# Kernel optimization log

Measured on AMD Instinct MI355X. Metric: run time of the kernel, lower is better.

Reference implementation:

```python
import jax, jax.numpy as jnp
import numpy as np

GAMMA_EXP = 1.0 / 2.2
PATTERN = 'RGGB'
H, W = 3072, 4096


def _conv1d(x, k, axis):
    """Cross-correlation of 2D x with 1D kernel k along axis, reflect padding
    (matches torch F.conv2d on reflect-padded input)."""
    p = (len(k) - 1) // 2
    pad = [(p, p) if a == axis else (0, 0) for a in range(2)]
    xp = jnp.pad(x, pad, mode='reflect')
    n = x.shape[axis]
    out = jnp.zeros_like(x)
    for i, ki in enumerate(k):
        if ki == 0.0:
            continue
        sl = [slice(None), slice(None)]
        sl[axis] = slice(i, i + n)
        out = out + ki * xp[tuple(sl)]
    return out


def _bayer_masks(shape, pattern):
    ch = {c: np.zeros((2, 2), np.float32) for c in 'RGB'}
    for i, c in enumerate(pattern):
        ch[c][i // 2, i % 2] = 1.0
    reps = ((shape[0] + 1) // 2, (shape[1] + 1) // 2)
    return tuple(jnp.asarray(np.tile(ch[c], reps)[:shape[0], :shape[1]]) for c in 'RGB')


def _shift_left2(x, axis):
    # pad by 2 on the far side with reflect, then drop first 2 -> x[j+2] with reflect at border
    pad = [(0, 2) if a == axis else (0, 0) for a in range(2)]
    xp = jnp.pad(x, pad, mode='reflect')
    sl = [slice(None), slice(None)]
    sl[axis] = slice(2, None)
    return xp[tuple(sl)]


def _menon2007(CFA, pattern):
    R_m, G_m, B_m = _bayer_masks(CFA.shape, pattern)
    h0 = [0.0, 0.5, 0.0, 0.5, 0.0]
    h1 = [-0.25, 0.0, 0.5, 0.0, -0.25]

    R = CFA * R_m
    G = CFA * G_m
    B = CFA * B_m

    G_H = jnp.where(G_m == 0, _conv1d(CFA, h0, 1) + _conv1d(CFA, h1, 1), G)
    G_V = jnp.where(G_m == 0, _conv1d(CFA, h0, 0) + _conv1d(CFA, h1, 0), G)

    C_H = jnp.where(R_m == 1, R - G_H, 0.0)
    C_H = jnp.where(B_m == 1, B - G_H, C_H)
    C_V = jnp.where(R_m == 1, R - G_V, 0.0)
    C_V = jnp.where(B_m == 1, B - G_V, C_V)

    D_H = jnp.abs(C_H - _shift_left2(C_H, axis=1))
    D_V = jnp.abs(C_V - _shift_left2(C_V, axis=0))

    k_row = [0.0, 0.0, 3.0, 0.0, 3.0]   # k[2, :]
    k_col = [1.0, 0.0, 3.0, 0.0, 1.0]   # k[:, 2]
    d_H = _conv1d(D_H, k_row, 1) + _conv1d(D_H, k_col, 0) - D_H * 3.0
    d_V = _conv1d(D_V, k_row, 1) + _conv1d(D_V, k_col, 0) - D_V * 3.0

    M = (d_V >= d_H).astype(CFA.dtype)
    G = jnp.where(G_m == 1, G, M * G_H + (1.0 - M) * G_V)

    R_r = jnp.any(R_m == 1, axis=1, keepdims=True) & jnp.ones_like(R_m, bool)
    B_r = jnp.any(B_m == 1, axis=1, keepdims=True) & jnp.ones_like(B_m, bool)
    kb = [0.5, 0.0, 0.5]

    R = jnp.where((G_m == 1) & R_r, G + _conv1d(R, kb, 1) - _conv1d(G, kb, 1), R)
    R = jnp.where((G_m == 1) & B_r, G + _conv1d(R, kb, 0) - _conv1d(G, kb, 0), R)
    B = jnp.where((G_m == 1) & B_r, G + _conv1d(B, kb, 1) - _conv1d(G, kb, 1), B)
    B = jnp.where((G_m == 1) & R_r, G + _conv1d(B, kb, 0) - _conv1d(G, kb, 0), B)

    R_at_B = M * (B + _conv1d(R, kb, 1) - _conv1d(B, kb, 1)) \
           + (1.0 - M) * (B + _conv1d(R, kb, 0) - _conv1d(B, kb, 0))
    R = jnp.where(B_r & (B_m == 1), R_at_B, R)

    B_at_R = M * (R + _conv1d(B, kb, 1) - _conv1d(R, kb, 1)) \
           + (1.0 - M) * (R + _conv1d(B, kb, 0) - _conv1d(R, kb, 0))
    B = jnp.where(R_r & (R_m == 1), B_at_R, B)

    return jnp.stack([R, G, B], axis=0)


def setup_inputs() -> dict:
    key = jax.random.key(0)
    k1, _ = jax.random.split(key)
    raw = jax.random.uniform(k1, (H, W), dtype=jnp.float32)
    wb = jnp.array([1.6, 1.2, 1.4], dtype=jnp.float32).reshape(3, 1, 1)
    return {"raw": raw, "wb": wb}


def reference(raw, wb):
    scaled = raw.astype(jnp.float32) / 65535.0
    rgb = _menon2007(scaled, PATTERN)
    rgb = rgb * wb
    rgb = jnp.clip(rgb, 0.0, 1.0)
    mn = jnp.min(rgb)
    mx = jnp.max(rgb)
    rng = mx - mn
    rgb = jnp.where(rng > 1e-6, (rgb - mn) / jnp.maximum(rng, 1e-12), rgb)
    rgb = jnp.power(jnp.maximum(rgb, 1e-12), GAMMA_EXP)
    return rgb
```

## Files before the change

### kernel.cpp

```cpp
#include <hip/hip_runtime.h>
#include <hip/hip_bf16.h>
#include <hip/hip_fp16.h>

#pragma clang fp contract(off)

constexpr int IMG_H = 3072;
constexpr int IMG_W = 4096;
constexpr int TS = 32;
constexpr float GAMMA_E = (float)(1.0 / 2.2);
constexpr float SC = 1048576.0f;
constexpr float INV_SC = 1.0f / SC;

__device__ __forceinline__ int mir(int v, int n) {
    v = (v < 0) ? -v : v;
    return (v >= n) ? (2 * n - 2 - v) : v;
}

constexpr int CFA_STR = 44, GH_STR = 40, GV_STR = 40, DH_STR = 40, DV_STR = 40,
              G_STR = 36, HV_STR = 36;
constexpr int OFF_CFA = 0;
constexpr int OFF_GH  = OFF_CFA + 46*44;
constexpr int OFF_GV  = OFF_GH  + 40*40;
constexpr int OFF_DH  = OFF_GV  + 42*40;
constexpr int OFF_DV  = OFF_DH  + 40*40;
constexpr int OFF_G   = OFF_DV  + 40*40;
constexpr int SMEM_N  = OFF_G   + 36*36;
constexpr int OFF_HH  = OFF_DH;
constexpr int OFF_VV  = OFF_DV;

__global__ void init_slots(unsigned int* slots) {
    int t = threadIdx.x;
    if (t < 512) slots[t] = (t < 256) ? 0x7F800000u : 0u;
}

__device__ __forceinline__ float pack_gm(float g, unsigned mb) {
    return __uint_as_float((__float_as_uint(g) & ~1u) | mb);
}

template <bool FP16>
__global__ __launch_bounds__(256) void demosaic_pass1(
    const float* __restrict__ raw, const float* __restrict__ wb,
    float* __restrict__ out, __half* __restrict__ hout,
    unsigned int* __restrict__ slots)
{
    __shared__ __align__(16) float sm[SMEM_N];
    __shared__ float redmn[4], redmx[4];
    const int tid = threadIdx.x;
    const int gr0 = blockIdx.y * TS;
    const int gc0 = blockIdx.x * TS;
    const bool fast = (blockIdx.x != 0) && (blockIdx.x != gridDim.x - 1) &&
                      (blockIdx.y != 0) && (blockIdx.y != gridDim.y - 1);

    if (fast) {
        const float* src = raw + (long long)(gr0 - 6) * IMG_W + (gc0 - 4);
        auto doLoad = [&](int ar, int q) {
            float4 v = *(const float4*)(src + ar * IMG_W + (q << 2));
            *(float4*)&sm[OFF_CFA + ar * CFA_STR + (q << 2)] =
                make_float4(v.x / 65535.0f, v.y / 65535.0f, v.z / 65535.0f, v.w / 65535.0f);
        };
        for (int i = tid; i < 368; i += 256) doLoad(i >> 3, i & 7);
        for (int i = tid; i < 138; i += 256) doLoad(i / 3, 8 + (i % 3));
        __syncthreads();

        auto doGH4 = [&](int ar, int ac4) {
            int cb = OFF_CFA + (ar + 2) * CFA_STR + ac4;
            const float4 a = *(const float4*)&sm[cb];
            const float4 b = *(const float4*)&sm[cb + 4];
            float w[8] = {a.x, a.y, a.z, a.w, b.x, b.y, b.z, b.w};
            float o[4];
#pragma unroll
            for (int j = 0; j < 4; ++j) {
                float x0 = w[j + 2];
                float t0 = 0.5f * w[j + 1] + 0.5f * w[j + 3];
                float t1 = (-0.25f * w[j] + 0.5f * x0) + (-0.25f * w[j + 4]);
                o[j] = ((ar + ac4 + j) & 1) ? x0 : (t0 + t1);
            }
            *(float4*)&sm[OFF_GH + ar * GH_STR + ac4] = make_float4(o[0], o[1], o[2], o[3]);
        };
        for (int i = tid; i < 320; i += 256) doGH4(i >> 3, (i & 7) << 2);
        for (int i = tid; i < 80; i += 256) doGH4(i >> 1, 32 + ((i & 1) << 2));

        auto doGV44 = [&](int rb, int ac4) {
            int r0 = (rb == 10) ? 38 : (rb << 2);
            float col[4][8];
#pragma unroll
            for (int k = 0; k < 8; ++k) {
                int rbase = OFF_CFA + (r0 + k) * CFA_STR + ac4;
                const float4 qa = *(const float4*)&sm[rbase];
                const float4 qb = *(const float4*)&sm[rbase + 4];
                col[0][k] = qa.z; col[1][k] = qa.w; col[2][k] = qb.x; col[3][k] = qb.y;
            }
#pragma unroll
            for (int ii = 0; ii < 4; ++ii) {
                float o[4];
#pragma unroll
                for (int j = 0; j < 4; ++j) {
                    float x0 = col[j][ii + 2];
                    float t0 = 0.5f * col[j][ii + 1] + 0.5f * col[j][ii + 3];
                    float t1 = (-0.25f * col[j][ii] + 0.5f * x0) + (-0.25f * col[j][ii + 4]);
                    o[j] = ((r0 + ii + ac4 + j) & 1) ? x0 : (t0 + t1);
                }
                *(float4*)&sm[OFF_GV + (r0 + ii) * GV_STR + ac4] = make_float4(o[0], o[1], o[2], o[3]);
            }
        };
        for (int i = tid; i < 88; i += 256) doGV44(i >> 3, (i & 7) << 2);
        for (int i = tid; i < 22; i += 256) doGV44(i >> 1, 32 + ((i & 1) << 2));
        __syncthreads();

        auto doD4 = [&](int ar, int ac4) {
            int cb = OFF_CFA + (ar + 2) * CFA_STR + ac4;
            const float4 a = *(const float4*)&sm[cb];
            const float4 b = *(const float4*)&sm[cb + 4];
            float cw[8] = {a.x, a.y, a.z, a.w, b.x, b.y, b.z, b.w};
            int c4b = OFF_CFA + (ar + 4) * CFA_STR + ac4;
            const float4 da = *(const float4*)&sm[c4b];
            const float4 db = *(const float4*)&sm[c4b + 4];
            float cd[4] = {da.z, da.w, db.x, db.y};
            const float4 g0 = *(const float4*)&sm[OFF_GH + ar * GH_STR + ac4];
            const float4 g1 = *(const float4*)&sm[OFF_GH + ar * GH_STR + ac4 + 4];
            float gh[8] = {g0.x, g0.y, g0.z, g0.w, g1.x, g1.y, g1.z, g1.w};
            const float4 v0 = *(const float4*)&sm[OFF_GV + ar * GV_STR + ac4];
            const float4 v2 = *(const float4*)&sm[OFF_GV + (ar + 2) * GV_STR + ac4];
            float gva[4] = {v0.x, v0.y, v0.z, v0.w};
            float gvb[4] = {v2.x, v2.y, v2.z, v2.w};
            float oh[4], ov[4];
#pragma unroll
            for (int j = 0; j < 4; ++j) {
                float aH = cw[j + 2] - gh[j];
                float bH = cw[j + 4] - gh[j + 2];
                oh[j] = fabsf(aH - bH);
                float aV = cw[j + 2] - gva[j];
                float bV = cd[j] - gvb[j];
                ov[j] = fabsf(aV - bV);
            }
            *(float4*)&sm[OFF_DH + ar * DH_STR + ac4] = make_float4(oh[0], oh[1], oh[2], oh[3]);
            *(float4*)&sm[OFF_DV + ar * DV_STR + ac4] = make_float4(ov[0], ov[1], ov[2], ov[3]);
        };
        for (int i = tid; i < 320; i += 256) doD4(i >> 3, (i & 7) << 2);
        for (int i = tid; i < 80; i += 256) doD4(i >> 1, 32 + ((i & 1) << 2));
        __syncthreads();

        auto doMG4 = [&](int ar, int ac4) {
            int hb2 = OFF_DH + (ar + 2) * DH_STR + ac4;
            const float4 h0 = *(const float4*)&sm[hb2];
            const float4 h1 = *(const float4*)&sm[hb2 + 4];
            float hw[8] = {h0.x, h0.y, h0.z, h0.w, h1.x, h1.y, h1.z, h1.w};
            const float4 huq = *(const float4*)&sm[OFF_DH + ar * DH_STR + ac4];
            const float4 hdq = *(const float4*)&sm[OFF_DH + (ar + 4) * DH_STR + ac4];
            int vb2 = OFF_DV + (ar + 2) * DV_STR + ac4;
            const float4 w0 = *(const float4*)&sm[vb2];
            const float4 w1 = *(const float4*)&sm[vb2 + 4];
            float vw[8] = {w0.x, w0.y, w0.z, w0.w, w1.x, w1.y, w1.z, w1.w};
            const float4 vuq = *(const float4*)&sm[OFF_DV + ar * DV_STR + ac4];
            const float4 vdq = *(const float4*)&sm[OFF_DV + (ar + 4) * DV_STR + ac4];
            float hu[4] = {huq.x, huq.y, huq.z, huq.w};
            float hd[4] = {hdq.x, hdq.y, hdq.z, hdq.w};
            float vu[4] = {vuq.x, vuq.y, vuq.z, vuq.w};
            float vd[4] = {vdq.x, vdq.y, vdq.z, vdq.w};
            int cfb = OFF_CFA + (ar + 4) * CFA_STR + ac4;
            const float4 ca = *(const float4*)&sm[cfb];
            const float4 cbq = *(const float4*)&sm[cfb + 4];
            float cf[4] = {ca.z, ca.w, cbq.x, cbq.y};
            const float4 ghq = *(const float4*)&sm[OFF_GH + (ar + 2) * GH_STR + ac4];
            const float4 gvq = *(const float4*)&sm[OFF_GV + (ar + 2) * GV_STR + ac4];
            float gha[4] = {ghq.x, ghq.y, ghq.z, ghq.w};
            float gvv[4] = {gvq.x, gvq.y, gvq.z, gvq.w};
            float o[4];
#pragma unroll
            for (int j = 0; j < 4; ++j) {
                float Dh0 = hw[j];
                float trowH = 3.0f * Dh0 + 3.0f * hw[j + 2];
                float tcolH = (hu[j] + 3.0f * Dh0) + hd[j];
                float dHv = (trowH + tcolH) - 3.0f * Dh0;
                float Dv0 = vw[j];
                float trowV = 3.0f * Dv0 + 3.0f * vw[j + 2];
                float tcolV = (vu[j] + 3.0f * Dv0) + vd[j];
                float dVv = (trowV + tcolV) - 3.0f * Dv0;
                unsigned mb = (dVv >= dHv) ? 1u : 0u;
                float g = ((ar + ac4 + j) & 1) ? cf[j] : (mb ? gha[j] : gvv[j]);
                o[j] = pack_gm(g, mb);
            }
            *(float4*)&sm[OFF_G + ar * G_STR + ac4] = make_float4(o[0], o[1], o[2], o[3]);
        };
        for (int i = tid; i < 288; i += 256) doMG4(i >> 3, (i & 7) << 2);
        for (int i = tid; i < 36; i += 256) doMG4(i, 32);
        __syncthreads();

        auto doHV4 = [&](int ar, int ac4) {
            int gb1 = OFF_G + (ar + 1) * G_STR + ac4;
            const float4 ga = *(const float4*)&sm[gb1];
            const float4 gb2 = *(const float4*)&sm[gb1 + 4];
            float gw[8] = {ga.x, ga.y, ga.z, ga.w, gb2.x, gb2.y, gb2.z, gb2.w};
            int gub = OFF_G + ar * G_STR + ac4;
            const float4 gua = *(const float4*)&sm[gub];
            const float4 gub4 = *(const float4*)&sm[gub + 4];
            float gu[6] = {gua.x, gua.y, gua.z, gua.w, gub4.x, gub4.y};
            int gdb = OFF_G + (ar + 2) * G_STR + ac4;
            const float4 gda = *(const float4*)&sm[gdb];
            const float4 gdb4 = *(const float4*)&sm[gdb + 4];
            float gd[6] = {gda.x, gda.y, gda.z, gda.w, gdb4.x, gdb4.y};
            int c5 = OFF_CFA + (ar + 5) * CFA_STR + ac4;
            const float4 ca = *(const float4*)&sm[c5];
            const float4 cb2 = *(const float4*)&sm[c5 + 4];
            float cw[8] = {ca.x, ca.y, ca.z, ca.w, cb2.x, cb2.y, cb2.z, cb2.w};
            int c4i = OFF_CFA + (ar + 4) * CFA_STR + ac4;
            const float4 cua = *(const float4*)&sm[c4i];
            const float4 cub = *(const float4*)&sm[c4i + 4];
            float cu[8] = {cua.x, cua.y, cua.z, cua.w, cub.x, cub.y, cub.z, cub.w};
            int c6i = OFF_CFA + (ar + 6) * CFA_STR + ac4;
            const float4 cda = *(const float4*)&sm[c6i];
            const float4 cdb = *(const float4*)&sm[c6i + 4];
            float cdn[8] = {cda.x, cda.y, cda.z, cda.w, cdb.x, cdb.y, cdb.z, cdb.w};
            float oh[4], ov[4];
#pragma unroll
            for (int j = 0; j < 4; ++j) {
                float g0 = gw[j + 1];
                oh[j] = g0 + 0.5f * (cw[j + 2] + cw[j + 4] - gw[j] - gw[j + 2]);
                ov[j] = g0 + 0.5f * (cu[j + 3] + cdn[j + 3] - gu[j + 1] - gd[j + 1]);
            }
            *(float4*)&sm[OFF_HH + ar * HV_STR + ac4] = make_float4(oh[0], oh[1], oh[2], oh[3]);
            *(float4*)&sm[OFF_VV + ar * HV_STR + ac4] = make_float4(ov[0], ov[1], ov[2], ov[3]);
        };
        for (int i = tid; i < 272; i += 256) doHV4(i >> 3, (i & 7) << 2);
        for (int i = tid; i < 34; i += 256) doHV4(i, 32);
    } else {
        auto CFA = [&](int r, int c) -> float { return sm[OFF_CFA + (r - gr0 + 6) * CFA_STR + (c - gc0 + 4)]; };
        auto GH  = [&](int r, int c) -> float { return sm[OFF_GH  + (r - gr0 + 4) * GH_STR  + (c - gc0 + 2)]; };
        auto GV  = [&](int r, int c) -> float { return sm[OFF_GV  + (r - gr0 + 4) * GV_STR  + (c - gc0 + 2)]; };
        auto DH  = [&](int r, int c) -> float { return sm[OFF_DH  + (r - gr0 + 4) * DH_STR  + (c - gc0 + 2)]; };
        auto DV  = [&](int r, int c) -> float { return sm[OFF_DV  + (r - gr0 + 4) * DV_STR  + (c - gc0 + 2)]; };
        auto Gg  = [&](int r, int c) -> float { return sm[OFF_G   + (r - gr0 + 2) * G_STR   + (c - gc0 + 2)]; };

        for (int i = tid; i < 46 * 44; i += 256) {
            int ar = i / 44, ac = i % 44;
            int r2 = mir(gr0 + ar - 6, IMG_H), c2 = mir(gc0 + ac - 4, IMG_W);
            sm[OFF_CFA + ar * CFA_STR + ac] = raw[r2 * IMG_W + c2] / 65535.0f;
        }
        __syncthreads();
        for (int i = tid; i < 40 * 40; i += 256) {
            int ar = i / 40, ac = i % 40;
            int r2 = mir(gr0 + ar - 4, IMG_H), c2 = mir(gc0 + ac - 2, IMG_W);
            float x0 = CFA(r2, c2);
            float t0 = 0.5f * CFA(r2, c2 - 1) + 0.5f * CFA(r2, c2 + 1);
            float t1 = (-0.25f * CFA(r2, c2 - 2) + 0.5f * x0) + (-0.25f * CFA(r2, c2 + 2));
            sm[OFF_GH + ar * GH_STR + ac] = (((r2 + c2) & 1) ? x0 : (t0 + t1));
        }
        for (int i = tid; i < 42 * 38; i += 256) {
            int ar = i / 38, ac = i % 38;
            int r2 = mir(gr0 + ar - 4, IMG_H), c2 = mir(gc0 + ac - 2, IMG_W);
            float x0 = CFA(r2, c2);
            float t0 = 0.5f * CFA(r2 - 1, c2) + 0.5f * CFA(r2 + 1, c2);
            float t1 = (-0.25f * CFA(r2 - 2, c2) + 0.5f * x0) + (-0.25f * CFA(r2 + 2, c2));
            sm[OFF_GV + ar * GV_STR + ac] = (((r2 + c2) & 1) ? x0 : (t0 + t1));
        }
        __syncthreads();
        for (int i = tid; i < 40 * 38; i += 256) {
            int ar = i / 38, ac = i % 38;
            int r2 = mir(gr0 + ar - 4, IMG_H), c2 = mir(gc0 + ac - 2, IMG_W);
            float aH = CFA(r2, c2) - GH(r2, c2);
            float bH = CFA(r2, c2 + 2) - GH(r2, c2 + 2);
            float aV = CFA(r2, c2) - GV(r2, c2);
            float bV = CFA(r2 + 2, c2) - GV(r2 + 2, c2);
            sm[OFF_DH + ar * DH_STR + ac] = fabsf(aH - bH);
            sm[OFF_DV + ar * DV_STR + ac] = fabsf(aV - bV);
        }
        __syncthreads();
        for (int i = tid; i < 36 * 36; i += 256) {
            int ar = i / 36, ac = i % 36;
            int r2 = mir(gr0 + ar - 2, IMG_H), c2 = mir(gc0 + ac - 2, IMG_W);
            float Dh0 = DH(r2, c2);
            float trowH = 3.0f * Dh0 + 3.0f * DH(r2, c2 + 2);
            float tcolH = (DH(r2 - 2, c2) + 3.0f * Dh0) + DH(r2 + 2, c2);
            float dHv = (trowH + tcolH) - 3.0f * Dh0;
            float Dv0 = DV(r2, c2);
            float trowV = 3.0f * Dv0 + 3.0f * DV(r2, c2 + 2);
            float tcolV = (DV(r2 - 2, c2) + 3.0f * Dv0) + DV(r2 + 2, c2);
            float dVv = (trowV + tcolV) - 3.0f * Dv0;
            unsigned mb = (dVv >= dHv) ? 1u : 0u;
            float g = ((r2 + c2) & 1) ? CFA(r2, c2) : (mb ? GH(r2, c2) : GV(r2, c2));
            sm[OFF_G + ar * G_STR + ac] = pack_gm(g, mb);
        }
        __syncthreads();
        for (int i = tid; i < 34 * 34; i += 256) {
            int ar = i / 34, ac = i % 34;
            int r2 = mir(gr0 + ar - 1, IMG_H), c2 = mir(gc0 + ac - 1, IMG_W);
            float g0 = Gg(r2, c2);
            float hh = g0 + 0.5f * (CFA(r2, c2 - 1) + CFA(r2, c2 + 1) - Gg(r2, c2 - 1) - Gg(r2, c2 + 1));
            float vv = g0 + 0.5f * (CFA(r2 - 1, c2) + CFA(r2 + 1, c2) - Gg(r2 - 1, c2) - Gg(r2 + 1, c2));
            sm[OFF_HH + ar * HV_STR + ac] = hh;
            sm[OFF_VV + ar * HV_STR + ac] = vv;
        }
    }
    __syncthreads();

    const float wr = wb[0], wg = wb[1], wbv = wb[2];
    const int pr = tid >> 3;
    const int pc0 = (tid & 7) << 2;
    const bool rowOdd = (pr & 1) != 0;
    int hbase = OFF_HH + (pr + 1) * HV_STR + pc0;
    const float4 h1a = *(const float4*)&sm[hbase];
    const float4 h1b = *(const float4*)&sm[hbase + 4];
    float hwc[8] = {h1a.x, h1a.y, h1a.z, h1a.w, h1b.x, h1b.y, h1b.z, h1b.w};
    int vbase = OFF_VV + (pr + 1) * HV_STR + pc0;
    const float4 v1a = *(const float4*)&sm[vbase];
    const float4 v1b = *(const float4*)&sm[vbase + 4];
    float vwc[8] = {v1a.x, v1a.y, v1a.z, v1a.w, v1b.x, v1b.y, v1b.z, v1b.w};
    int hub = OFF_HH + pr * HV_STR + pc0;
    const float4 huA = *(const float4*)&sm[hub];
    const float4 huB = *(const float4*)&sm[hub + 4];
    float hu[6] = {huA.x, huA.y, huA.z, huA.w, huB.x, huB.y};
    int hdb = OFF_HH + (pr + 2) * HV_STR + pc0;
    const float4 hdA = *(const float4*)&sm[hdb];
    const float4 hdB = *(const float4*)&sm[hdb + 4];
    float hd[6] = {hdA.x, hdA.y, hdA.z, hdA.w, hdB.x, hdB.y};
    int vub = OFF_VV + pr * HV_STR + pc0;
    const float4 vuA = *(const float4*)&sm[vub];
    const float4 vuB = *(const float4*)&sm[vub + 4];
    float vu[6] = {vuA.x, vuA.y, vuA.z, vuA.w, vuB.x, vuB.y};
    int vdb = OFF_VV + (pr + 2) * HV_STR + pc0;
    const float4 vdA = *(const float4*)&sm[vdb];
    const float4 vdB = *(const float4*)&sm[vdb + 4];
    float vd[6] = {vdA.x, vdA.y, vdA.z, vdA.w, vdB.x, vdB.y};
    const float4 cfq = *(const float4*)&sm[OFF_CFA + (pr + 6) * CFA_STR + pc0 + 4];
    float cf[4] = {cfq.x, cfq.y, cfq.z, cfq.w};
    int ggb = OFF_G + (pr + 2) * G_STR + pc0;
    const float4 gA = *(const float4*)&sm[ggb];
    const float4 gB = *(const float4*)&sm[ggb + 4];
    float ggr[4] = {gA.z, gA.w, gB.x, gB.y};

    float mn = 1e30f, mx = -1e30f;
    float rr[4], go[4], bo[4];
    __half hR[4], hG[4], hB[4];
#pragma unroll
    for (int j = 0; j < 4; ++j) {
        const float cfa = cf[j];
        const float g = ggr[j];
        const unsigned mb = __float_as_uint(g) & 1u;
        float sH = (hwc[j] - vwc[j]) + (hwc[j + 2] - vwc[j + 2]);
        float sV = (hu[j + 1] - vu[j + 1]) + (hd[j + 1] - vd[j + 1]);
        float X = mb ? (cfa - 0.5f * sH) : (cfa + 0.5f * sV);
        float R, B;
        if ((j & 1) == 0) {
            R = rowOdd ? vwc[j + 1] : cfa;
            B = rowOdd ? hwc[j + 1] : X;
        } else {
            R = rowOdd ? X : hwc[j + 1];
            B = rowOdd ? cfa : vwc[j + 1];
        }
        R = fminf(fmaxf(R * wr, 0.f), 1.f);
        float Gx = fminf(fmaxf(g * wg, 0.f), 1.f);
        B = fminf(fmaxf(B * wbv, 0.f), 1.f);
        if constexpr (FP16) {
            hR[j] = __float2half(R * SC);  R  = __half2float(hR[j]);
            hG[j] = __float2half(Gx * SC); Gx = __half2float(hG[j]);
            hB[j] = __float2half(B * SC);  B  = __half2float(hB[j]);
        }
        mn = fminf(mn, fminf(R, fminf(Gx, B)));
        mx = fmaxf(mx, fmaxf(R, fmaxf(Gx, B)));
        rr[j] = R; go[j] = Gx; bo[j] = B;
    }
    const long long HW = (long long)IMG_H * IMG_W;
    const long long base = (long long)(gr0 + pr) * IMG_W + (gc0 + pc0);
    if constexpr (FP16) {
        auto pack = [](__half a, __half b) {
            __half2 p = __halves2half2(a, b);
            return *reinterpret_cast<unsigned int*>(&p);
        };
        *(uint2*)(hout + base)          = make_uint2(pack(hR[0], hR[1]), pack(hR[2], hR[3]));
        *(uint2*)(hout + HW + base)     = make_uint2(pack(hG[0], hG[1]), pack(hG[2], hG[3]));
        *(uint2*)(hout + 2 * HW + base) = make_uint2(pack(hB[0], hB[1]), pack(hB[2], hB[3]));
    } else {
        *(float4*)(out + base)          = make_float4(rr[0], rr[1], rr[2], rr[3]);
        *(float4*)(out + HW + base)     = make_float4(go[0], go[1], go[2], go[3]);
        *(float4*)(out + 2 * HW + base) = make_float4(bo[0], bo[1], bo[2], bo[3]);
    }

#pragma unroll
    for (int off2 = 32; off2 > 0; off2 >>= 1) {
        mn = fminf(mn, __shfl_xor(mn, off2));
        mx = fmaxf(mx, __shfl_xor(mx, off2));
    }
    if ((tid & 63) == 0) { redmn[tid >> 6] = mn; redmx[tid >> 6] = mx; }
    __syncthreads();
    if (tid == 0) {
        mn = fminf(fminf(redmn[0], redmn[1]), fminf(redmn[2], redmn[3]));
        mx = fmaxf(fmaxf(redmx[0], redmx[1]), fmaxf(redmx[2], redmx[3]));
        if constexpr (FP16) { mn *= INV_SC; mx *= INV_SC; }
        int slot = (int)((blockIdx.y * gridDim.x + blockIdx.x) & 255);
        atomicMin(&slots[slot], __float_as_uint(mn));
        atomicMax(&slots[256 + slot], __float_as_uint(mx));
    }
}

__device__ __forceinline__ void reduce_slots(const unsigned int* slots, int tid,
                                             float* smn, float* smx, float& mn, float& mx) {
    mn = __uint_as_float(slots[tid]);
    mx = __uint_as_float(slots[256 + tid]);
#pragma unroll
    for (int off2 = 32; off2 > 0; off2 >>= 1) {
        mn = fminf(mn, __shfl_xor(mn, off2));
        mx = fmaxf(mx, __shfl_xor(mx, off2));
    }
    if ((tid & 63) == 0) { smn[tid >> 6] = mn; smx[tid >> 6] = mx; }
    __syncthreads();
    mn = fminf(fminf(smn[0], smn[1]), fminf(smn[2], smn[3]));
    mx = fmaxf(fmaxf(smx[0], smx[1]), fmaxf(smx[2], smx[3]));
}

__device__ __forceinline__ float gamma_hw(float a) {
    return __builtin_amdgcn_exp2f(GAMMA_E * __builtin_amdgcn_logf(a));
}

__global__ __launch_bounds__(256) void finalize_pass2_h(
    const __half* __restrict__ hin, float* __restrict__ out,
    const unsigned int* __restrict__ slots)
{
    __shared__ float smn[4], smx[4];
    const int tid = threadIdx.x;
    float mn, mx;
    reduce_slots(slots, tid, smn, smx, mn, mx);
    const float rng = mx - mn;
    const bool app = rng > 1e-6f;
    const float invden = 1.0f / fmaxf(rng, 1e-12f);

    const long long n8 = (long long)3 * IMG_H * IMG_W / 8;
    const uint4* pin = (const uint4*)hin;
    float4* po = (float4*)out;
    for (long long idx = (long long)blockIdx.x * blockDim.x + tid; idx < n8;
         idx += (long long)gridDim.x * blockDim.x) {
        uint4 u = pin[idx];
        float f[8];
        float2 t;
        t = __half22float2(*(__half2*)&u.x); f[0] = t.x; f[1] = t.y;
        t = __half22float2(*(__half2*)&u.y); f[2] = t.x; f[3] = t.y;
        t = __half22float2(*(__half2*)&u.z); f[4] = t.x; f[5] = t.y;
        t = __half22float2(*(__half2*)&u.w); f[6] = t.x; f[7] = t.y;
#pragma unroll
        for (int k = 0; k < 8; ++k) {
            float a = f[k] * INV_SC;
            a = app ? (a - mn) * invden : a;
            f[k] = gamma_hw(fmaxf(a, 1e-12f));
        }
        po[2 * idx]     = make_float4(f[0], f[1], f[2], f[3]);
        po[2 * idx + 1] = make_float4(f[4], f[5], f[6], f[7]);
    }
}

__global__ __launch_bounds__(256) void finalize_pass2_f(
    float* __restrict__ out, const unsigned int* __restrict__ slots)
{
    __shared__ float smn[4], smx[4];
    const int tid = threadIdx.x;
    float mn, mx;
    reduce_slots(slots, tid, smn, smx, mn, mx);
    const float rng = mx - mn;
    const bool app = rng > 1e-6f;
    const float invden = 1.0f / fmaxf(rng, 1e-12f);

    const long long n4 = (long long)3 * IMG_H * IMG_W / 4;
    float4* p = (float4*)out;
    for (long long idx = (long long)blockIdx.x * blockDim.x + tid; idx < n4;
         idx += (long long)gridDim.x * blockDim.x) {
        float4 v = p[idx];
        v.x = gamma_hw(fmaxf(app ? (v.x - mn) * invden : v.x, 1e-12f));
        v.y = gamma_hw(fmaxf(app ? (v.y - mn) * invden : v.y, 1e-12f));
        v.z = gamma_hw(fmaxf(app ? (v.z - mn) * invden : v.z, 1e-12f));
        v.w = gamma_hw(fmaxf(app ? (v.w - mn) * invden : v.w, 1e-12f));
        p[idx] = v;
    }
}

extern "C" void kernel_launch(void* const* d_in, const int* in_sizes, int n_in,
                              void* d_out, int out_size, void* d_ws, size_t ws_size,
                              hipStream_t stream) {
    (void)in_sizes; (void)n_in; (void)out_size;
    const float* raw = (const float*)d_in[0];
    const float* wb = (const float*)d_in[1];
    float* out = (float*)d_out;
    unsigned int* slots = (unsigned int*)d_ws;
    __half* hplanes = (__half*)((char*)d_ws + 4096);
    const size_t need = 4096 + (size_t)3 * IMG_H * IMG_W * sizeof(__half);
    const bool use_fp16 = ws_size >= need;

    init_slots<<<1, 512, 0, stream>>>(slots);
    dim3 grid(IMG_W / TS, IMG_H / TS);
    if (use_fp16) {
        demosaic_pass1<true><<<grid, 256, 0, stream>>>(raw, wb, out, hplanes, slots);
        finalize_pass2_h<<<dim3(2048), 256, 0, stream>>>(hplanes, out, slots);
    } else {
        demosaic_pass1<false><<<grid, 256, 0, stream>>>(raw, wb, out, hplanes, slots);
        finalize_pass2_f<<<dim3(2048), 256, 0, stream>>>(out, slots);
    }
}
```

Baseline: 177.9 us.

## Fuse G_H/G_V into D computation and store only non-green D values

The separate G_H and G_V shared-memory stages are removed. The horizontal and vertical green estimates are recomputed on the fly in the D stage and in the M/G stage, and D_H and D_V are stored only at non-green sites in a half-width layout. This removes two shared arrays and one barrier and shrinks the LDS footprint, with launch bounds requesting 6 blocks per CU for higher occupancy. In exchange it adds redundant arithmetic, plus parity-dependent indexing and more register pressure.

```diff
diff --git a/kernel.cpp b/kernel.cpp
--- a/kernel.cpp
+++ b/kernel.cpp
@@ -16,17 +16,17 @@
     return (v >= n) ? (2 * n - 2 - v) : v;
 }
 
-constexpr int CFA_STR = 44, GH_STR = 40, GV_STR = 40, DH_STR = 40, DV_STR = 40,
-              G_STR = 36, HV_STR = 36;
+constexpr int CFA_STR = 44;
+constexpr int D_STR   = 20;
+constexpr int G_STR   = 36;
+constexpr int HV_STR  = 36;
 constexpr int OFF_CFA = 0;
-constexpr int OFF_GH  = OFF_CFA + 46*44;
-constexpr int OFF_GV  = OFF_GH  + 40*40;
-constexpr int OFF_DH  = OFF_GV  + 42*40;
-constexpr int OFF_DV  = OFF_DH  + 40*40;
-constexpr int OFF_G   = OFF_DV  + 40*40;
-constexpr int SMEM_N  = OFF_G   + 36*36;
+constexpr int OFF_G   = 2024;
+constexpr int OFF_DH  = OFF_G + 36*36;
+constexpr int OFF_DV  = OFF_DH + 40*20;
 constexpr int OFF_HH  = OFF_DH;
-constexpr int OFF_VV  = OFF_DV;
+constexpr int OFF_VV  = OFF_HH + 34*36;
+constexpr int SMEM_N  = OFF_VV + 34*36;
 
 __global__ void init_slots(unsigned int* slots) {
     int t = threadIdx.x;
@@ -38,7 +38,7 @@
 }
 
 template <bool FP16>
-__global__ __launch_bounds__(256) void demosaic_pass1(
+__global__ __launch_bounds__(256, 6) void demosaic_pass1(
     const float* __restrict__ raw, const float* __restrict__ wb,
     float* __restrict__ out, __half* __restrict__ hout,
     unsigned int* __restrict__ slots)
@@ -53,183 +53,212 @@
 
     if (fast) {
         const float* src = raw + (long long)(gr0 - 6) * IMG_W + (gc0 - 4);
-        auto doLoad = [&](int ar, int q) {
-            float4 v = *(const float4*)(src + ar * IMG_W + (q << 2));
-            *(float4*)&sm[OFF_CFA + ar * CFA_STR + (q << 2)] =
+        auto doLoad = [&](int ar, int qd) {
+            float4 v = *(const float4*)(src + ar * IMG_W + (qd << 2));
+            *(float4*)&sm[OFF_CFA + ar * CFA_STR + (qd << 2)] =
                 make_float4(v.x / 65535.0f, v.y / 65535.0f, v.z / 65535.0f, v.w / 65535.0f);
         };
         for (int i = tid; i < 368; i += 256) doLoad(i >> 3, i & 7);
         for (int i = tid; i < 138; i += 256) doLoad(i / 3, 8 + (i % 3));
         __syncthreads();
 
-        auto doGH4 = [&](int ar, int ac4) {
-            int cb = OFF_CFA + (ar + 2) * CFA_STR + ac4;
-            const float4 a = *(const float4*)&sm[cb];
-            const float4 b = *(const float4*)&sm[cb + 4];
-            float w[8] = {a.x, a.y, a.z, a.w, b.x, b.y, b.z, b.w};
-            float o[4];
+        auto doA = [&](int ar, int ku) {
+            const int p = ar & 1;
+            const int cb = OFF_CFA + (ar + 2) * CFA_STR + 8 * ku;
+            float w[16];
+            {
+                const float4 a = *(const float4*)&sm[cb];
+                const float4 b = *(const float4*)&sm[cb + 4];
+                const float4 c = *(const float4*)&sm[cb + 8];
+                const float4 d = *(const float4*)&sm[cb + 12];
+                w[0]=a.x; w[1]=a.y; w[2]=a.z; w[3]=a.w;
+                w[4]=b.x; w[5]=b.y; w[6]=b.z; w[7]=b.w;
+                w[8]=c.x; w[9]=c.y; w[10]=c.z; w[11]=c.w;
+                w[12]=d.x; w[13]=d.y; w[14]=d.z; w[15]=d.w;
+            }
+            float cvj[7][4];
+#pragma unroll
+            for (int k = 0; k < 7; ++k) {
+                if (k == 2) {
+                    cvj[2][0]=w[2+p]; cvj[2][1]=w[4+p]; cvj[2][2]=w[6+p]; cvj[2][3]=w[8+p];
+                    continue;
+                }
+                int rb = OFF_CFA + (ar + k) * CFA_STR + 8 * ku;
+                float2 e  = *(const float2*)&sm[rb + 2];
+                float4 f  = *(const float4*)&sm[rb + 4];
+                float2 g2 = *(const float2*)&sm[rb + 8];
+                if (p == 0) { cvj[k][0]=e.x; cvj[k][1]=f.x; cvj[k][2]=f.z; cvj[k][3]=g2.x; }
+                else        { cvj[k][0]=e.y; cvj[k][1]=f.y; cvj[k][2]=f.w; cvj[k][3]=g2.y; }
+            }
+            auto ghe = [&](int wi) -> float {
+                float x0 = w[wi];
+                float t0 = 0.5f * w[wi-1] + 0.5f * w[wi+1];
+                float t1 = (-0.25f * w[wi-2] + 0.5f * x0) + (-0.25f * w[wi+2]);
+                return t0 + t1;
+            };
+            auto gve = [&](int k0, int j2) -> float {
+                float x0 = cvj[k0][j2];
+                float t0 = 0.5f * cvj[k0-1][j2] + 0.5f * cvj[k0+1][j2];
+                float t1 = (-0.25f * cvj[k0-2][j2] + 0.5f * x0) + (-0.25f * cvj[k0+2][j2]);
+                return t0 + t1;
+            };
+            float dhp[4], dvp[4];
 #pragma unroll
             for (int j = 0; j < 4; ++j) {
-                float x0 = w[j + 2];
-                float t0 = 0.5f * w[j + 1] + 0.5f * w[j + 3];
-                float t1 = (-0.25f * w[j] + 0.5f * x0) + (-0.25f * w[j + 4]);
-                o[j] = ((ar + ac4 + j) & 1) ? x0 : (t0 + t1);
-            }
-            *(float4*)&sm[OFF_GH + ar * GH_STR + ac4] = make_float4(o[0], o[1], o[2], o[3]);
-        };
-        for (int i = tid; i < 320; i += 256) doGH4(i >> 3, (i & 7) << 2);
-        for (int i = tid; i < 80; i += 256) doGH4(i >> 1, 32 + ((i & 1) << 2));
-
-        auto doGV44 = [&](int rb, int ac4) {
-            int r0 = (rb == 10) ? 38 : (rb << 2);
-            float col[4][8];
-#pragma unroll
-            for (int k = 0; k < 8; ++k) {
-                int rbase = OFF_CFA + (r0 + k) * CFA_STR + ac4;
-                const float4 qa = *(const float4*)&sm[rbase];
-                const float4 qb = *(const float4*)&sm[rbase + 4];
-                col[0][k] = qa.z; col[1][k] = qa.w; col[2][k] = qb.x; col[3][k] = qb.y;
-            }
-#pragma unroll
-            for (int ii = 0; ii < 4; ++ii) {
-                float o[4];
-#pragma unroll
-                for (int j = 0; j < 4; ++j) {
-                    float x0 = col[j][ii + 2];
-                    float t0 = 0.5f * col[j][ii + 1] + 0.5f * col[j][ii + 3];
-                    float t1 = (-0.25f * col[j][ii] + 0.5f * x0) + (-0.25f * col[j][ii + 4]);
-                    o[j] = ((r0 + ii + ac4 + j) & 1) ? x0 : (t0 + t1);
+                int wi = 2*j + 2 + p;
+                float gh0 = ghe(wi), gh2 = ghe(wi + 2);
+                float ch0 = w[wi] - gh0, ch2 = w[wi + 2] - gh2;
+                dhp[j] = fabsf(ch0 - ch2);
+                float gv0 = gve(2, j), gv2 = gve(4, j);
+                float cv0 = cvj[2][j] - gv0, cv2 = cvj[4][j] - gv2;
+                dvp[j] = fabsf(cv0 - cv2);
+            }
+            *(float4*)&sm[OFF_DH + ar * D_STR + 4*ku] = make_float4(dhp[0],dhp[1],dhp[2],dhp[3]);
+            *(float4*)&sm[OFF_DV + ar * D_STR + 4*ku] = make_float4(dvp[0],dvp[1],dvp[2],dvp[3]);
+        };
+        for (int i = tid; i < 200; i += 256) doA(i / 5, i % 5);
+        __syncthreads();
+
+        auto doB = [&](int ar, int ku) {
+            const int q = ar & 1;
+            const int k4 = 4 * ku;
+            float hw[6], vw[6], hu[4], hd[4], vu[4], vd[4];
+            {
+                int b0 = OFF_DH + (ar + 2) * D_STR + k4;
+                float4 t = *(const float4*)&sm[b0]; hw[0]=t.x; hw[1]=t.y; hw[2]=t.z; hw[3]=t.w;
+                float2 u = *(const float2*)&sm[b0 + 4]; hw[4]=u.x; hw[5]=u.y;
+                float4 a = *(const float4*)&sm[OFF_DH + ar*D_STR + k4];     hu[0]=a.x; hu[1]=a.y; hu[2]=a.z; hu[3]=a.w;
+                float4 b = *(const float4*)&sm[OFF_DH + (ar+4)*D_STR + k4]; hd[0]=b.x; hd[1]=b.y; hd[2]=b.z; hd[3]=b.w;
+                int v0 = OFF_DV + (ar + 2) * D_STR + k4;
+                float4 t2 = *(const float4*)&sm[v0]; vw[0]=t2.x; vw[1]=t2.y; vw[2]=t2.z; vw[3]=t2.w;
+                float2 u2 = *(const float2*)&sm[v0 + 4]; vw[4]=u2.x; vw[5]=u2.y;
+                float4 a2 = *(const float4*)&sm[OFF_DV + ar*D_STR + k4];     vu[0]=a2.x; vu[1]=a2.y; vu[2]=a2.z; vu[3]=a2.w;
+                float4 b2 = *(const float4*)&sm[OFF_DV + (ar+4)*D_STR + k4]; vd[0]=b2.x; vd[1]=b2.y; vd[2]=b2.z; vd[3]=b2.w;
+            }
+            const int cb2 = OFF_CFA + (ar + 4) * CFA_STR + 8 * ku;
+            float w2[16];
+            {
+                const float4 a = *(const float4*)&sm[cb2];
+                const float4 b = *(const float4*)&sm[cb2 + 4];
+                const float4 c = *(const float4*)&sm[cb2 + 8];
+                const float4 d = *(const float4*)&sm[cb2 + 12];
+                w2[0]=a.x; w2[1]=a.y; w2[2]=a.z; w2[3]=a.w;
+                w2[4]=b.x; w2[5]=b.y; w2[6]=b.z; w2[7]=b.w;
+                w2[8]=c.x; w2[9]=c.y; w2[10]=c.z; w2[11]=c.w;
+                w2[12]=d.x; w2[13]=d.y; w2[14]=d.z; w2[15]=d.w;
+            }
+            float cwj[5][4];
+#pragma unroll
+            for (int k = 0; k < 5; ++k) {
+                if (k == 2) {
+                    cwj[2][0]=w2[2+q]; cwj[2][1]=w2[4+q]; cwj[2][2]=w2[6+q]; cwj[2][3]=w2[8+q];
+                    continue;
                 }
-                *(float4*)&sm[OFF_GV + (r0 + ii) * GV_STR + ac4] = make_float4(o[0], o[1], o[2], o[3]);
-            }
-        };
-        for (int i = tid; i < 88; i += 256) doGV44(i >> 3, (i & 7) << 2);
-        for (int i = tid; i < 22; i += 256) doGV44(i >> 1, 32 + ((i & 1) << 2));
-        __syncthreads();
-
-        auto doD4 = [&](int ar, int ac4) {
-            int cb = OFF_CFA + (ar + 2) * CFA_STR + ac4;
-            const float4 a = *(const float4*)&sm[cb];
-            const float4 b = *(const float4*)&sm[cb + 4];
-            float cw[8] = {a.x, a.y, a.z, a.w, b.x, b.y, b.z, b.w};
-            int c4b = OFF_CFA + (ar + 4) * CFA_STR + ac4;
-            const float4 da = *(const float4*)&sm[c4b];
-            const float4 db = *(const float4*)&sm[c4b + 4];
-            float cd[4] = {da.z, da.w, db.x, db.y};
-            const float4 g0 = *(const float4*)&sm[OFF_GH + ar * GH_STR + ac4];
-            const float4 g1 = *(const float4*)&sm[OFF_GH + ar * GH_STR + ac4 + 4];
-            float gh[8] = {g0.x, g0.y, g0.z, g0.w, g1.x, g1.y, g1.z, g1.w};
-            const float4 v0 = *(const float4*)&sm[OFF_GV + ar * GV_STR + ac4];
-            const float4 v2 = *(const float4*)&sm[OFF_GV + (ar + 2) * GV_STR + ac4];
-            float gva[4] = {v0.x, v0.y, v0.z, v0.w};
-            float gvb[4] = {v2.x, v2.y, v2.z, v2.w};
-            float oh[4], ov[4];
-#pragma unroll
-            for (int j = 0; j < 4; ++j) {
-                float aH = cw[j + 2] - gh[j];
-                float bH = cw[j + 4] - gh[j + 2];
-                oh[j] = fabsf(aH - bH);
-                float aV = cw[j + 2] - gva[j];
-                float bV = cd[j] - gvb[j];
-                ov[j] = fabsf(aV - bV);
-            }
-            *(float4*)&sm[OFF_DH + ar * DH_STR + ac4] = make_float4(oh[0], oh[1], oh[2], oh[3]);
-            *(float4*)&sm[OFF_DV + ar * DV_STR + ac4] = make_float4(ov[0], ov[1], ov[2], ov[3]);
-        };
-        for (int i = tid; i < 320; i += 256) doD4(i >> 3, (i & 7) << 2);
-        for (int i = tid; i < 80; i += 256) doD4(i >> 1, 32 + ((i & 1) << 2));
-        __syncthreads();
-
-        auto doMG4 = [&](int ar, int ac4) {
-            int hb2 = OFF_DH + (ar + 2) * DH_STR + ac4;
-            const float4 h0 = *(const float4*)&sm[hb2];
-            const float4 h1 = *(const float4*)&sm[hb2 + 4];
-            float hw[8] = {h0.x, h0.y, h0.z, h0.w, h1.x, h1.y, h1.z, h1.w};
-            const float4 huq = *(const float4*)&sm[OFF_DH + ar * DH_STR + ac4];
-            const float4 hdq = *(const float4*)&sm[OFF_DH + (ar + 4) * DH_STR + ac4];
-            int vb2 = OFF_DV + (ar + 2) * DV_STR + ac4;
-            const float4 w0 = *(const float4*)&sm[vb2];
-            const float4 w1 = *(const float4*)&sm[vb2 + 4];
-            float vw[8] = {w0.x, w0.y, w0.z, w0.w, w1.x, w1.y, w1.z, w1.w};
-            const float4 vuq = *(const float4*)&sm[OFF_DV + ar * DV_STR + ac4];
-            const float4 vdq = *(const float4*)&sm[OFF_DV + (ar + 4) * DV_STR + ac4];
-            float hu[4] = {huq.x, huq.y, huq.z, huq.w};
-            float hd[4] = {hdq.x, hdq.y, hdq.z, hdq.w};
-            float vu[4] = {vuq.x, vuq.y, vuq.z, vuq.w};
-            float vd[4] = {vdq.x, vdq.y, vdq.z, vdq.w};
-            int cfb = OFF_CFA + (ar + 4) * CFA_STR + ac4;
-            const float4 ca = *(const float4*)&sm[cfb];
-            const float4 cbq = *(const float4*)&sm[cfb + 4];
-            float cf[4] = {ca.z, ca.w, cbq.x, cbq.y};
-            const float4 ghq = *(const float4*)&sm[OFF_GH + (ar + 2) * GH_STR + ac4];
-            const float4 gvq = *(const float4*)&sm[OFF_GV + (ar + 2) * GV_STR + ac4];
-            float gha[4] = {ghq.x, ghq.y, ghq.z, ghq.w};
-            float gvv[4] = {gvq.x, gvq.y, gvq.z, gvq.w};
-            float o[4];
+                int rb = OFF_CFA + (ar + 2 + k) * CFA_STR + 8 * ku;
+                float2 e  = *(const float2*)&sm[rb + 2];
+                float4 f  = *(const float4*)&sm[rb + 4];
+                float2 g2 = *(const float2*)&sm[rb + 8];
+                if (q == 0) { cwj[k][0]=e.x; cwj[k][1]=f.x; cwj[k][2]=f.z; cwj[k][3]=g2.x; }
+                else        { cwj[k][0]=e.y; cwj[k][1]=f.y; cwj[k][2]=f.w; cwj[k][3]=g2.y; }
+            }
+            auto ghe2 = [&](int wi) -> float {
+                float x0 = w2[wi];
+                float t0 = 0.5f * w2[wi-1] + 0.5f * w2[wi+1];
+                float t1 = (-0.25f * w2[wi-2] + 0.5f * x0) + (-0.25f * w2[wi+2]);
+                return t0 + t1;
+            };
+            auto gve2 = [&](int j2) -> float {
+                float x0 = cwj[2][j2];
+                float t0 = 0.5f * cwj[1][j2] + 0.5f * cwj[3][j2];
+                float t1 = (-0.25f * cwj[0][j2] + 0.5f * x0) + (-0.25f * cwj[4][j2]);
+                return t0 + t1;
+            };
+            float gnb[4];
 #pragma unroll
             for (int j = 0; j < 4; ++j) {
                 float Dh0 = hw[j];
-                float trowH = 3.0f * Dh0 + 3.0f * hw[j + 2];
-                float tcolH = (hu[j] + 3.0f * Dh0) + hd[j];
-                float dHv = (trowH + tcolH) - 3.0f * Dh0;
+                float trowH = 3.0f*Dh0 + 3.0f*hw[j+1];
+                float tcolH = (hu[j] + 3.0f*Dh0) + hd[j];
+                float dH = (trowH + tcolH) - 3.0f*Dh0;
                 float Dv0 = vw[j];
-                float trowV = 3.0f * Dv0 + 3.0f * vw[j + 2];
-                float tcolV = (vu[j] + 3.0f * Dv0) + vd[j];
-                float dVv = (trowV + tcolV) - 3.0f * Dv0;
-                unsigned mb = (dVv >= dHv) ? 1u : 0u;
-                float g = ((ar + ac4 + j) & 1) ? cf[j] : (mb ? gha[j] : gvv[j]);
-                o[j] = pack_gm(g, mb);
-            }
-            *(float4*)&sm[OFF_G + ar * G_STR + ac4] = make_float4(o[0], o[1], o[2], o[3]);
-        };
-        for (int i = tid; i < 288; i += 256) doMG4(i >> 3, (i & 7) << 2);
-        for (int i = tid; i < 36; i += 256) doMG4(i, 32);
-        __syncthreads();
-
-        auto doHV4 = [&](int ar, int ac4) {
-            int gb1 = OFF_G + (ar + 1) * G_STR + ac4;
-            const float4 ga = *(const float4*)&sm[gb1];
-            const float4 gb2 = *(const float4*)&sm[gb1 + 4];
-            float gw[8] = {ga.x, ga.y, ga.z, ga.w, gb2.x, gb2.y, gb2.z, gb2.w};
-            int gub = OFF_G + ar * G_STR + ac4;
-            const float4 gua = *(const float4*)&sm[gub];
-            const float4 gub4 = *(const float4*)&sm[gub + 4];
-            float gu[6] = {gua.x, gua.y, gua.z, gua.w, gub4.x, gub4.y};
-            int gdb = OFF_G + (ar + 2) * G_STR + ac4;
-            const float4 gda = *(const float4*)&sm[gdb];
-            const float4 gdb4 = *(const float4*)&sm[gdb + 4];
-            float gd[6] = {gda.x, gda.y, gda.z, gda.w, gdb4.x, gdb4.y};
-            int c5 = OFF_CFA + (ar + 5) * CFA_STR + ac4;
-            const float4 ca = *(const float4*)&sm[c5];
-            const float4 cb2 = *(const float4*)&sm[c5 + 4];
-            float cw[8] = {ca.x, ca.y, ca.z, ca.w, cb2.x, cb2.y, cb2.z, cb2.w};
-            int c4i = OFF_CFA + (ar + 4) * CFA_STR + ac4;
-            const float4 cua = *(const float4*)&sm[c4i];
-            const float4 cub = *(const float4*)&sm[c4i + 4];
-            float cu[8] = {cua.x, cua.y, cua.z, cua.w, cub.x, cub.y, cub.z, cub.w};
-            int c6i = OFF_CFA + (ar + 6) * CFA_STR + ac4;
-            const float4 cda = *(const float4*)&sm[c6i];
-            const float4 cdb = *(const float4*)&sm[c6i + 4];
-            float cdn[8] = {cda.x, cda.y, cda.z, cda.w, cdb.x, cdb.y, cdb.z, cdb.w};
+                float trowV = 3.0f*Dv0 + 3.0f*vw[j+1];
+                float tcolV = (vu[j] + 3.0f*Dv0) + vd[j];
+                float dV = (trowV + tcolV) - 3.0f*Dv0;
+                unsigned mb = (dV >= dH) ? 1u : 0u;
+                float gsel = mb ? ghe2(2*j + 2 + q) : gve2(j);
+                gnb[j] = pack_gm(gsel, mb);
+            }
+            int gb = OFF_G + ar * G_STR + 8 * ku;
+            if (q == 0) {
+                *(float4*)&sm[gb] = make_float4(gnb[0], w2[3], gnb[1], w2[5]);
+                if (ku < 4) *(float4*)&sm[gb+4] = make_float4(gnb[2], w2[7], gnb[3], w2[9]);
+            } else {
+                *(float4*)&sm[gb] = make_float4(w2[2], gnb[0], w2[4], gnb[1]);
+                if (ku < 4) *(float4*)&sm[gb+4] = make_float4(w2[6], gnb[2], w2[8], gnb[3]);
+            }
+        };
+        for (int i = tid; i < 180; i += 256) doB(i / 5, i % 5);
+        __syncthreads();
+
+        auto doC = [&](int ar, int hc4) {
+            const float4 gmA = *(const float4*)&sm[OFF_G + (ar+1)*G_STR + hc4];
+            const float4 gmB = *(const float4*)&sm[OFF_G + (ar+1)*G_STR + hc4 + 4];
+            float gm[8] = {gmA.x,gmA.y,gmA.z,gmA.w, gmB.x,gmB.y,gmB.z,gmB.w};
+            const float4 guA = *(const float4*)&sm[OFF_G + ar*G_STR + hc4];
+            const float4 guB = *(const float4*)&sm[OFF_G + ar*G_STR + hc4 + 4];
+            float gu[8] = {guA.x,guA.y,guA.z,guA.w, guB.x,guB.y,guB.z,guB.w};
+            const float4 gdA = *(const float4*)&sm[OFF_G + (ar+2)*G_STR + hc4];
+            const float4 gdB = *(const float4*)&sm[OFF_G + (ar+2)*G_STR + hc4 + 4];
+            float gd[8] = {gdA.x,gdA.y,gdA.z,gdA.w, gdB.x,gdB.y,gdB.z,gdB.w};
+            int c5 = OFF_CFA + (ar + 5) * CFA_STR + hc4;
+            const float4 w5A = *(const float4*)&sm[c5];
+            const float4 w5B = *(const float4*)&sm[c5 + 4];
+            float w5[8] = {w5A.x,w5A.y,w5A.z,w5A.w, w5B.x,w5B.y,w5B.z,w5B.w};
+            int c4i = OFF_CFA + (ar + 4) * CFA_STR + hc4;
+            const float4 w4A = *(const float4*)&sm[c4i];
+            const float4 w4B = *(const float4*)&sm[c4i + 4];
+            float w4[8] = {w4A.x,w4A.y,w4A.z,w4A.w, w4B.x,w4B.y,w4B.z,w4B.w};
+            int c6i = OFF_CFA + (ar + 6) * CFA_STR + hc4;
+            const float4 w6A = *(const float4*)&sm[c6i];
+            const float4 w6B = *(const float4*)&sm[c6i + 4];
+            float w6[8] = {w6A.x,w6A.y,w6A.z,w6A.w, w6B.x,w6B.y,w6B.z,w6B.w};
             float oh[4], ov[4];
 #pragma unroll
             for (int j = 0; j < 4; ++j) {
-                float g0 = gw[j + 1];
-                oh[j] = g0 + 0.5f * (cw[j + 2] + cw[j + 4] - gw[j] - gw[j + 2]);
-                ov[j] = g0 + 0.5f * (cu[j + 3] + cdn[j + 3] - gu[j + 1] - gd[j + 1]);
-            }
-            *(float4*)&sm[OFF_HH + ar * HV_STR + ac4] = make_float4(oh[0], oh[1], oh[2], oh[3]);
-            *(float4*)&sm[OFF_VV + ar * HV_STR + ac4] = make_float4(ov[0], ov[1], ov[2], ov[3]);
-        };
-        for (int i = tid; i < 272; i += 256) doHV4(i >> 3, (i & 7) << 2);
-        for (int i = tid; i < 34; i += 256) doHV4(i, 32);
+                float g0 = gm[j + 1];
+                oh[j] = g0 + 0.5f * (w5[j + 2] + w5[j + 4] - gm[j] - gm[j + 2]);
+                ov[j] = g0 + 0.5f * (w4[j + 3] + w6[j + 3] - gu[j + 1] - gd[j + 1]);
+            }
+            *(float4*)&sm[OFF_HH + ar * HV_STR + hc4] = make_float4(oh[0],oh[1],oh[2],oh[3]);
+            *(float4*)&sm[OFF_VV + ar * HV_STR + hc4] = make_float4(ov[0],ov[1],ov[2],ov[3]);
+        };
+        for (int i = tid; i < 272; i += 256) doC(i >> 3, (i & 7) << 2);
+        for (int i = tid; i < 34; i += 256) doC(i, 32);
     } else {
-        auto CFA = [&](int r, int c) -> float { return sm[OFF_CFA + (r - gr0 + 6) * CFA_STR + (c - gc0 + 4)]; };
-        auto GH  = [&](int r, int c) -> float { return sm[OFF_GH  + (r - gr0 + 4) * GH_STR  + (c - gc0 + 2)]; };
-        auto GV  = [&](int r, int c) -> float { return sm[OFF_GV  + (r - gr0 + 4) * GV_STR  + (c - gc0 + 2)]; };
-        auto DH  = [&](int r, int c) -> float { return sm[OFF_DH  + (r - gr0 + 4) * DH_STR  + (c - gc0 + 2)]; };
-        auto DV  = [&](int r, int c) -> float { return sm[OFF_DV  + (r - gr0 + 4) * DV_STR  + (c - gc0 + 2)]; };
-        auto Gg  = [&](int r, int c) -> float { return sm[OFF_G   + (r - gr0 + 2) * G_STR   + (c - gc0 + 2)]; };
+        auto CFAb = [&](int r, int c) -> float { return sm[OFF_CFA + (r - gr0 + 6) * CFA_STR + (c - gc0 + 4)]; };
+        auto Gb   = [&](int r, int c) -> float { return sm[OFF_G   + (r - gr0 + 2) * G_STR   + (c - gc0 + 2)]; };
+        auto DHL  = [&](int r, int c) -> float {
+            int dr = r - gr0 + 4;
+            int kk = ((c - gc0 + 2) - (dr & 1)) >> 1;
+            return sm[OFF_DH + dr * D_STR + kk];
+        };
+        auto DVL  = [&](int r, int c) -> float {
+            int dr = r - gr0 + 4;
+            int kk = ((c - gc0 + 2) - (dr & 1)) >> 1;
+            return sm[OFF_DV + dr * D_STR + kk];
+        };
+        auto ghB = [&](int r, int c) -> float {
+            float x0 = CFAb(r, c);
+            float t0 = 0.5f * CFAb(r, c - 1) + 0.5f * CFAb(r, c + 1);
+            float t1 = (-0.25f * CFAb(r, c - 2) + 0.5f * x0) + (-0.25f * CFAb(r, c + 2));
+            return t0 + t1;
+        };
+        auto gvB = [&](int r, int c) -> float {
+            float x0 = CFAb(r, c);
+            float t0 = 0.5f * CFAb(r - 1, c) + 0.5f * CFAb(r + 1, c);
+            float t1 = (-0.25f * CFAb(r - 2, c) + 0.5f * x0) + (-0.25f * CFAb(r + 2, c));
+            return t0 + t1;
+        };
 
         for (int i = tid; i < 46 * 44; i += 256) {
             int ar = i / 44, ac = i % 44;
@@ -237,59 +266,52 @@
             sm[OFF_CFA + ar * CFA_STR + ac] = raw[r2 * IMG_W + c2] / 65535.0f;
         }
         __syncthreads();
-        for (int i = tid; i < 40 * 40; i += 256) {
-            int ar = i / 40, ac = i % 40;
-            int r2 = mir(gr0 + ar - 4, IMG_H), c2 = mir(gc0 + ac - 2, IMG_W);
-            float x0 = CFA(r2, c2);
-            float t0 = 0.5f * CFA(r2, c2 - 1) + 0.5f * CFA(r2, c2 + 1);
-            float t1 = (-0.25f * CFA(r2, c2 - 2) + 0.5f * x0) + (-0.25f * CFA(r2, c2 + 2));
-            sm[OFF_GH + ar * GH_STR + ac] = (((r2 + c2) & 1) ? x0 : (t0 + t1));
-        }
-        for (int i = tid; i < 42 * 38; i += 256) {
-            int ar = i / 38, ac = i % 38;
-            int r2 = mir(gr0 + ar - 4, IMG_H), c2 = mir(gc0 + ac - 2, IMG_W);
-            float x0 = CFA(r2, c2);
-            float t0 = 0.5f * CFA(r2 - 1, c2) + 0.5f * CFA(r2 + 1, c2);
-            float t1 = (-0.25f * CFA(r2 - 2, c2) + 0.5f * x0) + (-0.25f * CFA(r2 + 2, c2));
-            sm[OFF_GV + ar * GV_STR + ac] = (((r2 + c2) & 1) ? x0 : (t0 + t1));
-        }
-        __syncthreads();
-        for (int i = tid; i < 40 * 38; i += 256) {
-            int ar = i / 38, ac = i % 38;
-            int r2 = mir(gr0 + ar - 4, IMG_H), c2 = mir(gc0 + ac - 2, IMG_W);
-            float aH = CFA(r2, c2) - GH(r2, c2);
-            float bH = CFA(r2, c2 + 2) - GH(r2, c2 + 2);
-            float aV = CFA(r2, c2) - GV(r2, c2);
-            float bV = CFA(r2 + 2, c2) - GV(r2 + 2, c2);
-            sm[OFF_DH + ar * DH_STR + ac] = fabsf(aH - bH);
-            sm[OFF_DV + ar * DV_STR + ac] = fabsf(aV - bV);
+        for (int i = tid; i < 40 * 19; i += 256) {
+            int ar = i / 19, k = i % 19;
+            int q = ar & 1, dl = 2 * k + q;
+            int r2 = mir(gr0 + ar - 4, IMG_H), c2 = mir(gc0 + dl - 2, IMG_W);
+            float ch0 = CFAb(r2, c2) - ghB(r2, c2);
+            int c22 = mir(c2 + 2, IMG_W);
+            float ch2 = CFAb(r2, c22) - ghB(r2, c22);
+            sm[OFF_DH + ar * D_STR + k] = fabsf(ch0 - ch2);
+            float cv0 = CFAb(r2, c2) - gvB(r2, c2);
+            int r22 = mir(r2 + 2, IMG_H);
+            float cv2 = CFAb(r22, c2) - gvB(r22, c2);
+            sm[OFF_DV + ar * D_STR + k] = fabsf(cv0 - cv2);
         }
         __syncthreads();
         for (int i = tid; i < 36 * 36; i += 256) {
-            int ar = i / 36, ac = i % 36;
-            int r2 = mir(gr0 + ar - 2, IMG_H), c2 = mir(gc0 + ac - 2, IMG_W);
-            float Dh0 = DH(r2, c2);
-            float trowH = 3.0f * Dh0 + 3.0f * DH(r2, c2 + 2);
-            float tcolH = (DH(r2 - 2, c2) + 3.0f * Dh0) + DH(r2 + 2, c2);
-            float dHv = (trowH + tcolH) - 3.0f * Dh0;
-            float Dv0 = DV(r2, c2);
-            float trowV = 3.0f * Dv0 + 3.0f * DV(r2, c2 + 2);
-            float tcolV = (DV(r2 - 2, c2) + 3.0f * Dv0) + DV(r2 + 2, c2);
-            float dVv = (trowV + tcolV) - 3.0f * Dv0;
-            unsigned mb = (dVv >= dHv) ? 1u : 0u;
-            float g = ((r2 + c2) & 1) ? CFA(r2, c2) : (mb ? GH(r2, c2) : GV(r2, c2));
-            sm[OFF_G + ar * G_STR + ac] = pack_gm(g, mb);
+            int ar = i / 36, gc = i % 36;
+            int r2 = mir(gr0 + ar - 2, IMG_H), c2 = mir(gc0 + gc - 2, IMG_W);
+            float g;
+            if ((r2 + c2) & 1) {
+                g = CFAb(r2, c2);
+            } else {
+                float Dh0 = DHL(r2, c2);
+                float trowH = 3.0f * Dh0 + 3.0f * DHL(r2, c2 + 2);
+                float tcolH = (DHL(r2 - 2, c2) + 3.0f * Dh0) + DHL(r2 + 2, c2);
+                float dH = (trowH + tcolH) - 3.0f * Dh0;
+                float Dv0 = DVL(r2, c2);
+                float trowV = 3.0f * Dv0 + 3.0f * DVL(r2, c2 + 2);
+                float tcolV = (DVL(r2 - 2, c2) + 3.0f * Dv0) + DVL(r2 + 2, c2);
+                float dV = (trowV + tcolV) - 3.0f * Dv0;
+                unsigned mb = (dV >= dH) ? 1u : 0u;
+                float gsel = mb ? ghB(r2, c2) : gvB(r2, c2);
+                g = pack_gm(gsel, mb);
+            }
+            sm[OFF_G + ar * G_STR + gc] = g;
         }
         __syncthreads();
         for (int i = tid; i < 34 * 34; i += 256) {
             int ar = i / 34, ac = i % 34;
             int r2 = mir(gr0 + ar - 1, IMG_H), c2 = mir(gc0 + ac - 1, IMG_W);
-            float g0 = Gg(r2, c2);
-            float hh = g0 + 0.5f * (CFA(r2, c2 - 1) + CFA(r2, c2 + 1) - Gg(r2, c2 - 1) - Gg(r2, c2 + 1));
-            float vv = g0 + 0.5f * (CFA(r2 - 1, c2) + CFA(r2 + 1, c2) - Gg(r2 - 1, c2) - Gg(r2 + 1, c2));
+            float g0 = Gb(r2, c2);
+            float hh = g0 + 0.5f * (CFAb(r2, c2 - 1) + CFAb(r2, c2 + 1) - Gb(r2, c2 - 1) - Gb(r2, c2 + 1));
+            float vv = g0 + 0.5f * (CFAb(r2 - 1, c2) + CFAb(r2 + 1, c2) - Gb(r2 - 1, c2) - Gb(r2 + 1, c2));
             sm[OFF_HH + ar * HV_STR + ac] = hh;
             sm[OFF_VV + ar * HV_STR + ac] = vv;
         }
+        __syncthreads();
     }
     __syncthreads();
 
@@ -305,27 +327,22 @@
     const float4 v1a = *(const float4*)&sm[vbase];
     const float4 v1b = *(const float4*)&sm[vbase + 4];
     float vwc[8] = {v1a.x, v1a.y, v1a.z, v1a.w, v1b.x, v1b.y, v1b.z, v1b.w};
-    int hub = OFF_HH + pr * HV_STR + pc0;
-    const float4 huA = *(const float4*)&sm[hub];
-    const float4 huB = *(const float4*)&sm[hub + 4];
+    const float4 huA = *(const float4*)&sm[OFF_HH + pr * HV_STR + pc0];
+    const float4 huB = *(const float4*)&sm[OFF_HH + pr * HV_STR + pc0 + 4];
     float hu[6] = {huA.x, huA.y, huA.z, huA.w, huB.x, huB.y};
-    int hdb = OFF_HH + (pr + 2) * HV_STR + pc0;
-    const float4 hdA = *(const float4*)&sm[hdb];
-    const float4 hdB = *(const float4*)&sm[hdb + 4];
+    const float4 hdA = *(const float4*)&sm[OFF_HH + (pr + 2) * HV_STR + pc0];
+    const float4 hdB = *(const float4*)&sm[OFF_HH + (pr + 2) * HV_STR + pc0 + 4];
     float hd[6] = {hdA.x, hdA.y, hdA.z, hdA.w, hdB.x, hdB.y};
-    int vub = OFF_VV + pr * HV_STR + pc0;
-    const float4 vuA = *(const float4*)&sm[vub];
-    const float4 vuB = *(const float4*)&sm[vub + 4];
+    const float4 vuA = *(const float4*)&sm[OFF_VV + pr * HV_STR + pc0];
+    const float4 vuB = *(const float4*)&sm[OFF_VV + pr * HV_STR + pc0 + 4];
     float vu[6] = {vuA.x, vuA.y, vuA.z, vuA.w, vuB.x, vuB.y};
-    int vdb = OFF_VV + (pr + 2) * HV_STR + pc0;
-    const float4 vdA = *(const float4*)&sm[vdb];
-    const float4 vdB = *(const float4*)&sm[vdb + 4];
+    const float4 vdA = *(const float4*)&sm[OFF_VV + (pr + 2) * HV_STR + pc0];
+    const float4 vdB = *(const float4*)&sm[OFF_VV + (pr + 2) * HV_STR + pc0 + 4];
     float vd[6] = {vdA.x, vdA.y, vdA.z, vdA.w, vdB.x, vdB.y};
     const float4 cfq = *(const float4*)&sm[OFF_CFA + (pr + 6) * CFA_STR + pc0 + 4];
     float cf[4] = {cfq.x, cfq.y, cfq.z, cfq.w};
-    int ggb = OFF_G + (pr + 2) * G_STR + pc0;
-    const float4 gA = *(const float4*)&sm[ggb];
-    const float4 gB = *(const float4*)&sm[ggb + 4];
+    const float4 gA = *(const float4*)&sm[OFF_G + (pr + 2) * G_STR + pc0];
+    const float4 gB = *(const float4*)&sm[OFF_G + (pr + 2) * G_STR + pc0 + 4];
     float ggr[4] = {gA.z, gA.w, gB.x, gB.y};
 
     float mn = 1e30f, mx = -1e30f;
```

Measured after the change: 158.7 us. -10.8%, faster.
